# Kernel tuning notes

Hardware: AMD Instinct MI355X
Metric: run time of the kernel (lower is better)

## Reference

```python
import jax, jax.numpy as jnp
import numpy as np

N_NODES = 50000
N_EDGES = 640000
DIM = 128
BN_EPS = 1e-5
AGG_EPS = 1e-6


def setup_inputs() -> dict:
    key = jax.random.key(0)
    ks = jax.random.split(key, 32)
    s = 1.0 / np.sqrt(DIM)
    d = {}
    d["x"] = jax.random.normal(ks[0], (N_NODES, DIM), jnp.float32)
    d["e"] = jax.random.normal(ks[1], (N_EDGES, DIM), jnp.float32)
    # Linear layers A,B,C,D,E: weight [out,in], bias [out]
    for i, n in enumerate(["A", "B", "C", "D", "E"]):
        d[n + "w"] = jax.random.normal(ks[2 + 2 * i], (DIM, DIM), jnp.float32) * s
        d[n + "b"] = jax.random.normal(ks[3 + 2 * i], (DIM,), jnp.float32) * s
    # BatchNorm (eval mode) params / running stats for node and edge BN
    d["bn_x_gamma"] = 1.0 + 0.1 * jax.random.normal(ks[12], (DIM,), jnp.float32)
    d["bn_x_beta"] = 0.1 * jax.random.normal(ks[13], (DIM,), jnp.float32)
    d["bn_x_mean"] = 0.1 * jax.random.normal(ks[14], (DIM,), jnp.float32)
    d["bn_x_var"] = 0.5 + jax.random.uniform(ks[15], (DIM,), jnp.float32)
    d["bn_e_gamma"] = 1.0 + 0.1 * jax.random.normal(ks[16], (DIM,), jnp.float32)
    d["bn_e_beta"] = 0.1 * jax.random.normal(ks[17], (DIM,), jnp.float32)
    d["bn_e_mean"] = 0.1 * jax.random.normal(ks[18], (DIM,), jnp.float32)
    d["bn_e_var"] = 0.5 + jax.random.uniform(ks[19], (DIM,), jnp.float32)
    d["edge_index"] = jax.random.randint(ks[20], (2, N_EDGES), 0, N_NODES, dtype=jnp.int64)
    return d


def reference(x, e, Aw, Ab, Bw, Bb, Cw, Cb, Dw, Db, Ew, Eb,
              bn_x_gamma, bn_x_beta, bn_x_mean, bn_x_var,
              bn_e_gamma, bn_e_beta, bn_e_mean, bn_e_var,
              edge_index):
    # PyG default flow: x_j gathers from edge_index[0] (source),
    # x_i / aggregation index from edge_index[1] (target).
    src, dst = edge_index[0], edge_index[1]

    Ax = x @ Aw.T + Ab
    Bx = x @ Bw.T + Bb
    Ce = e @ Cw.T + Cb
    Dx = x @ Dw.T + Db
    Ex = x @ Ew.T + Eb

    # message: gated edge features
    e_ij = Dx[dst] + Ex[src] + Ce            # [n_edges, out_dim]
    sigma = jax.nn.sigmoid(e_ij)

    # aggregate: dual scatter-sum + divide
    num = jax.ops.segment_sum(sigma * Bx[src], dst, num_segments=N_NODES)
    den = jax.ops.segment_sum(sigma, dst, num_segments=N_NODES)
    aggr = num / (den + AGG_EPS)

    x_new = Ax + aggr                        # update()

    # BatchNorm (eval, running stats) + relu; dropout p=0 in eval
    x_bn = (x_new - bn_x_mean) * jax.lax.rsqrt(bn_x_var + BN_EPS) * bn_x_gamma + bn_x_beta
    e_bn = (e_ij - bn_e_mean) * jax.lax.rsqrt(bn_e_var + BN_EPS) * bn_e_gamma + bn_e_beta

    x_out = x + jax.nn.relu(x_bn)            # residual
    e_out = e + jax.nn.relu(e_bn)            # residual
    return x_out, e_out
```

## Files before the change

kernel.cpp:

```cpp
#include <hip/hip_runtime.h>
#include <hip/hip_bf16.h>
#include <math.h>

#define N_NODES 50000
#define N_EDGES 640000
#define DIM 128
#define LDP 136

typedef __attribute__((ext_vector_type(8))) short short8;
typedef __attribute__((ext_vector_type(4))) float floatx4;

__device__ __forceinline__ unsigned short f2bf(float f) {
    unsigned int u = __float_as_uint(f);
    u += 0x7FFFu + ((u >> 16) & 1u);
    return (unsigned short)(u >> 16);
}
__device__ __forceinline__ float bf2f(unsigned short h) {
    return __uint_as_float(((unsigned int)h) << 16);
}

__global__ __launch_bounds__(256) void node_gemm(
    const float* __restrict__ x,
    const float* __restrict__ w0, const float* __restrict__ b0,
    const float* __restrict__ w1, const float* __restrict__ b1,
    const float* __restrict__ w2, const float* __restrict__ b2,
    const float* __restrict__ w3, const float* __restrict__ b3,
    float* __restrict__ o0, float* __restrict__ o1,
    float* __restrict__ o2, float* __restrict__ o3)
{
    __shared__ unsigned short Xs[64 * LDP];
    __shared__ unsigned short Ws[128 * LDP];
    const int tid  = threadIdx.x;
    const int mblk = blockIdx.x * 64;
    const int mid  = blockIdx.y;
    const float* W = mid == 0 ? w0 : mid == 1 ? w1 : mid == 2 ? w2 : w3;
    const float* B = mid == 0 ? b0 : mid == 1 ? b1 : mid == 2 ? b2 : b3;
    float*       O = mid == 0 ? o0 : mid == 1 ? o1 : mid == 2 ? o2 : o3;

#pragma unroll
    for (int i = 0; i < 8; ++i) {
        int slot = tid + i * 256;
        int row = slot >> 5, c4 = (slot & 31) << 2;
        int rg = mblk + row;
        float4 v = make_float4(0.f, 0.f, 0.f, 0.f);
        if (rg < N_NODES) v = *(const float4*)(x + (size_t)rg * DIM + c4);
        unsigned short* p = &Xs[row * LDP + c4];
        p[0] = f2bf(v.x); p[1] = f2bf(v.y); p[2] = f2bf(v.z); p[3] = f2bf(v.w);
    }
#pragma unroll
    for (int i = 0; i < 16; ++i) {
        int slot = tid + i * 256;
        int row = slot >> 5, c4 = (slot & 31) << 2;
        float4 v = *(const float4*)(W + row * DIM + c4);
        unsigned short* p = &Ws[row * LDP + c4];
        p[0] = f2bf(v.x); p[1] = f2bf(v.y); p[2] = f2bf(v.z); p[3] = f2bf(v.w);
    }
    __syncthreads();

    const int wave = tid >> 6, lane = tid & 63;
    const int q = lane >> 4, r = lane & 15;
    floatx4 acc[8];
#pragma unroll
    for (int i = 0; i < 8; ++i) acc[i] = (floatx4)(0.f);
    const int arow = wave * 16 + r;
#pragma unroll
    for (int kk = 0; kk < 4; ++kk) {
        short8 a = *(const short8*)&Xs[arow * LDP + kk * 32 + q * 8];
#pragma unroll
        for (int nt = 0; nt < 8; ++nt) {
            short8 b = *(const short8*)&Ws[(nt * 16 + r) * LDP + kk * 32 + q * 8];
            acc[nt] = __builtin_amdgcn_mfma_f32_16x16x32_bf16(a, b, acc[nt], 0, 0, 0);
        }
    }
#pragma unroll
    for (int nt = 0; nt < 8; ++nt) {
        int col = nt * 16 + r;
        float bv = B[col];
#pragma unroll
        for (int reg = 0; reg < 4; ++reg) {
            int rg = mblk + wave * 16 + q * 4 + reg;
            if (rg < N_NODES) O[(size_t)rg * DIM + col] = acc[nt][reg] + bv;
        }
    }
}

__global__ __launch_bounds__(256) void edge_kernel(
    const float* __restrict__ e,
    const float* __restrict__ Cw, const float* __restrict__ Cb,
    const int* __restrict__ ei,
    const float* __restrict__ Dx, const float* __restrict__ Ex,
    const float* __restrict__ Bx,
    const float* __restrict__ g,  const float* __restrict__ bt,
    const float* __restrict__ mn, const float* __restrict__ vr,
    float* __restrict__ num, float* __restrict__ den,
    float* __restrict__ e_out)
{
    __shared__ unsigned short Es[64 * LDP];
    __shared__ unsigned short Ws[128 * LDP];
    __shared__ int srcS[64], dstS[64];
    const int tid  = threadIdx.x;
    const int mblk = blockIdx.x * 64;

    if (tid < 64) {
        srcS[tid] = ei[mblk + tid];
        dstS[tid] = ei[N_EDGES + mblk + tid];
    }
#pragma unroll
    for (int i = 0; i < 8; ++i) {
        int slot = tid + i * 256;
        int row = slot >> 5, c4 = (slot & 31) << 2;
        float4 v = *(const float4*)(e + (size_t)(mblk + row) * DIM + c4);
        unsigned short* p = &Es[row * LDP + c4];
        p[0] = f2bf(v.x); p[1] = f2bf(v.y); p[2] = f2bf(v.z); p[3] = f2bf(v.w);
    }
#pragma unroll
    for (int i = 0; i < 16; ++i) {
        int slot = tid + i * 256;
        int row = slot >> 5, c4 = (slot & 31) << 2;
        float4 v = *(const float4*)(Cw + row * DIM + c4);
        unsigned short* p = &Ws[row * LDP + c4];
        p[0] = f2bf(v.x); p[1] = f2bf(v.y); p[2] = f2bf(v.z); p[3] = f2bf(v.w);
    }
    __syncthreads();

    const int wave = tid >> 6, lane = tid & 63;
    const int q = lane >> 4, r = lane & 15;
    floatx4 acc[8];
#pragma unroll
    for (int i = 0; i < 8; ++i) acc[i] = (floatx4)(0.f);
    const int arow = wave * 16 + r;
#pragma unroll
    for (int kk = 0; kk < 4; ++kk) {
        short8 a = *(const short8*)&Es[arow * LDP + kk * 32 + q * 8];
#pragma unroll
        for (int nt = 0; nt < 8; ++nt) {
            short8 b = *(const short8*)&Ws[(nt * 16 + r) * LDP + kk * 32 + q * 8];
            acc[nt] = __builtin_amdgcn_mfma_f32_16x16x32_bf16(a, b, acc[nt], 0, 0, 0);
        }
    }

#pragma unroll
    for (int nt = 0; nt < 8; ++nt) {
        int col = nt * 16 + r;
        float cb = Cb[col];
        float sc = g[col] * rsqrtf(vr[col] + 1e-5f);
        float sh = bt[col] - mn[col] * sc;
#pragma unroll
        for (int reg = 0; reg < 4; ++reg) {
            int rl = wave * 16 + q * 4 + reg;
            int rg = mblk + rl;
            int dd = dstS[rl], ss = srcS[rl];
            float eij = acc[nt][reg] + cb
                      + Dx[(size_t)dd * DIM + col] + Ex[(size_t)ss * DIM + col];
            float sg = 1.f / (1.f + __expf(-eij));
            atomicAdd(&num[(size_t)dd * DIM + col], sg * Bx[(size_t)ss * DIM + col]);
            atomicAdd(&den[(size_t)dd * DIM + col], sg);
            float bn = eij * sc + sh;
            e_out[(size_t)rg * DIM + col] = bf2f(Es[rl * LDP + col]) + (bn > 0.f ? bn : 0.f);
        }
    }
}

__global__ __launch_bounds__(256) void node_final(
    const float* __restrict__ x,  const float* __restrict__ Ax,
    const float* __restrict__ num, const float* __restrict__ den,
    const float* __restrict__ g,  const float* __restrict__ bt,
    const float* __restrict__ mn, const float* __restrict__ vr,
    float* __restrict__ x_out)
{
    int idx = (blockIdx.x * 256 + threadIdx.x) * 4;
    float4 a  = *(const float4*)(Ax + idx);
    float4 nm = *(const float4*)(num + idx);
    float4 dn = *(const float4*)(den + idx);
    float4 xv = *(const float4*)(x + idx);
    int col = idx & (DIM - 1);
    float av[4] = {a.x, a.y, a.z, a.w};
    float nv[4] = {nm.x, nm.y, nm.z, nm.w};
    float dv[4] = {dn.x, dn.y, dn.z, dn.w};
    float xs[4] = {xv.x, xv.y, xv.z, xv.w};
    float ov[4];
#pragma unroll
    for (int j = 0; j < 4; ++j) {
        float sc = g[col + j] * rsqrtf(vr[col + j] + 1e-5f);
        float sh = bt[col + j] - mn[col + j] * sc;
        float v = av[j] + nv[j] / (dv[j] + 1e-6f);
        float bn = v * sc + sh;
        ov[j] = xs[j] + (bn > 0.f ? bn : 0.f);
    }
    *(float4*)(x_out + idx) = make_float4(ov[0], ov[1], ov[2], ov[3]);
}

extern "C" void kernel_launch(void* const* d_in, const int* in_sizes, int n_in,
                              void* d_out, int out_size, void* d_ws, size_t ws_size,
                              hipStream_t stream) {
    const float* x  = (const float*)d_in[0];
    const float* e  = (const float*)d_in[1];
    const float* Aw = (const float*)d_in[2];  const float* Ab = (const float*)d_in[3];
    const float* Bw = (const float*)d_in[4];  const float* Bb = (const float*)d_in[5];
    const float* Cw = (const float*)d_in[6];  const float* Cb = (const float*)d_in[7];
    const float* Dw = (const float*)d_in[8];  const float* Db = (const float*)d_in[9];
    const float* Ew = (const float*)d_in[10]; const float* Eb = (const float*)d_in[11];
    const float* gx = (const float*)d_in[12]; const float* btx = (const float*)d_in[13];
    const float* mnx = (const float*)d_in[14]; const float* vrx = (const float*)d_in[15];
    const float* ge = (const float*)d_in[16]; const float* bte = (const float*)d_in[17];
    const float* mne = (const float*)d_in[18]; const float* vre = (const float*)d_in[19];
    const int*   ei = (const int*)d_in[20];

    const size_t NF = (size_t)N_NODES * DIM;
    float* ws  = (float*)d_ws;
    float* Ax  = ws;
    float* Bx  = ws + NF;
    float* Dx  = ws + 2 * NF;
    float* Ex  = ws + 3 * NF;
    float* num = ws + 4 * NF;
    float* den = ws + 5 * NF;

    float* x_out = (float*)d_out;
    float* e_out = x_out + NF;

    hipMemsetAsync(num, 0, 2 * NF * sizeof(float), stream);

    dim3 g1((N_NODES + 63) / 64, 4);
    node_gemm<<<g1, 256, 0, stream>>>(x, Aw, Ab, Bw, Bb, Dw, Db, Ew, Eb, Ax, Bx, Dx, Ex);

    edge_kernel<<<N_EDGES / 64, 256, 0, stream>>>(e, Cw, Cb, ei, Dx, Ex, Bx,
                                                  ge, bte, mne, vre, num, den, e_out);

    node_final<<<(int)(NF / 4 / 256), 256, 0, stream>>>(x, Ax, num, den,
                                                        gx, btx, mnx, vrx, x_out);
}
```

Measured before the change: 1.206 ms.

## Replace atomic scatter-sum with CSR gather aggregation and pre-converted bf16 operands

Builds a destination-sorted CSR (histogram, scan, position assignment) so the edge kernel writes sigmoid values to sorted slots. A per-node kernel then gathers and reduces numerator and denominator without float atomics. It also pre-converts x and the weights to bf16 once. The trade-off is an extra large sigma buffer in workspace, several extra small kernels, and a fallback to the old atomic path when the workspace is too small.

```diff
diff --git a/kernel.cpp b/kernel.cpp
--- a/kernel.cpp
+++ b/kernel.cpp
@@ -19,7 +19,282 @@
     return __uint_as_float(((unsigned int)h) << 16);
 }
 
-__global__ __launch_bounds__(256) void node_gemm(
+
+__global__ __launch_bounds__(256) void convert_x(
+    const float* __restrict__ x, unsigned short* __restrict__ xb)
+{
+    size_t i = (size_t)(blockIdx.x * 256 + threadIdx.x) * 8;
+    float4 a = *(const float4*)(x + i);
+    float4 b = *(const float4*)(x + i + 4);
+    short8 v;
+    v[0] = (short)f2bf(a.x); v[1] = (short)f2bf(a.y);
+    v[2] = (short)f2bf(a.z); v[3] = (short)f2bf(a.w);
+    v[4] = (short)f2bf(b.x); v[5] = (short)f2bf(b.y);
+    v[6] = (short)f2bf(b.z); v[7] = (short)f2bf(b.w);
+    *(short8*)(xb + i) = v;
+}
+
+__global__ __launch_bounds__(256) void convert_w(
+    const float* __restrict__ w0, const float* __restrict__ w1,
+    const float* __restrict__ w2, const float* __restrict__ w3,
+    const float* __restrict__ w4, unsigned short* __restrict__ wb)
+{
+    const float* W = blockIdx.y == 0 ? w0 : blockIdx.y == 1 ? w1 :
+                     blockIdx.y == 2 ? w2 : blockIdx.y == 3 ? w3 : w4;
+    int i = (blockIdx.x * 256 + threadIdx.x) * 8;
+    float4 a = *(const float4*)(W + i);
+    float4 b = *(const float4*)(W + i + 4);
+    short8 v;
+    v[0] = (short)f2bf(a.x); v[1] = (short)f2bf(a.y);
+    v[2] = (short)f2bf(a.z); v[3] = (short)f2bf(a.w);
+    v[4] = (short)f2bf(b.x); v[5] = (short)f2bf(b.y);
+    v[6] = (short)f2bf(b.z); v[7] = (short)f2bf(b.w);
+    *(short8*)(wb + (size_t)blockIdx.y * DIM * DIM + i) = v;
+}
+
+__global__ __launch_bounds__(256) void hist_kernel(
+    const int* __restrict__ ei, int* __restrict__ deg)
+{
+    int e = blockIdx.x * 256 + threadIdx.x;
+    atomicAdd(&deg[ei[N_EDGES + e]], 1);
+}
+
+__global__ __launch_bounds__(256) void scan1(
+    const int* __restrict__ deg, int* __restrict__ off, int* __restrict__ bsum)
+{
+    __shared__ int s[256];
+    int tid = threadIdx.x;
+    int i = blockIdx.x * 256 + tid;
+    int v = (i < N_NODES) ? deg[i] : 0;
+    s[tid] = v;
+    __syncthreads();
+#pragma unroll
+    for (int d = 1; d < 256; d <<= 1) {
+        int t = (tid >= d) ? s[tid - d] : 0;
+        __syncthreads();
+        s[tid] += t;
+        __syncthreads();
+    }
+    if (i < N_NODES) off[i] = s[tid] - v;
+    if (tid == 255) bsum[blockIdx.x] = s[tid];
+}
+
+__global__ __launch_bounds__(256) void scan2(int* __restrict__ bsum)
+{
+    __shared__ int s[256];
+    int tid = threadIdx.x;
+    int v = (tid < 196) ? bsum[tid] : 0;
+    s[tid] = v;
+    __syncthreads();
+#pragma unroll
+    for (int d = 1; d < 256; d <<= 1) {
+        int t = (tid >= d) ? s[tid - d] : 0;
+        __syncthreads();
+        s[tid] += t;
+        __syncthreads();
+    }
+    if (tid < 196) bsum[tid] = s[tid] - v;
+}
+
+__global__ __launch_bounds__(256) void scan3(
+    int* __restrict__ off, const int* __restrict__ bsum, int* __restrict__ cursor)
+{
+    int i = blockIdx.x * 256 + threadIdx.x;
+    if (i < N_NODES) {
+        int o = off[i] + bsum[blockIdx.x];
+        off[i] = o;
+        cursor[i] = o;
+    }
+    if (i == 0) off[N_NODES] = N_EDGES;
+}
+
+__global__ __launch_bounds__(256) void pos_kernel(
+    const int* __restrict__ ei, int* __restrict__ cursor,
+    int* __restrict__ pos, int* __restrict__ srcp)
+{
+    int e = blockIdx.x * 256 + threadIdx.x;
+    int d = ei[N_EDGES + e];
+    int s = ei[e];
+    int p = atomicAdd(&cursor[d], 1);
+    pos[e] = p;
+    srcp[p] = s;
+}
+
+__global__ __launch_bounds__(256) void node_gemm_bf(
+    const unsigned short* __restrict__ xb, const unsigned short* __restrict__ wb,
+    const float* __restrict__ b0, const float* __restrict__ b1,
+    const float* __restrict__ b2, const float* __restrict__ b3,
+    float* __restrict__ o0, float* __restrict__ o1,
+    float* __restrict__ o2, float* __restrict__ o3)
+{
+    __shared__ unsigned short Xs[64 * LDP];
+    __shared__ unsigned short Ws[128 * LDP];
+    const int tid  = threadIdx.x;
+    const int mblk = blockIdx.x * 64;
+    const int mid  = blockIdx.y;
+    const int widx = (mid < 2) ? mid : mid + 1;
+    const unsigned short* Wm = wb + (size_t)widx * DIM * DIM;
+    const float* B = mid == 0 ? b0 : mid == 1 ? b1 : mid == 2 ? b2 : b3;
+    float*       O = mid == 0 ? o0 : mid == 1 ? o1 : mid == 2 ? o2 : o3;
+
+#pragma unroll
+    for (int i = 0; i < 4; ++i) {
+        int slot = tid + i * 256;
+        int row = slot >> 4, c8 = (slot & 15) << 3;
+        int rg = mblk + row;
+        short8 v = (short8)(0);
+        if (rg < N_NODES) v = *(const short8*)(xb + (size_t)rg * DIM + c8);
+        *(short8*)&Xs[row * LDP + c8] = v;
+    }
+#pragma unroll
+    for (int i = 0; i < 8; ++i) {
+        int slot = tid + i * 256;
+        int row = slot >> 4, c8 = (slot & 15) << 3;
+        *(short8*)&Ws[row * LDP + c8] = *(const short8*)(Wm + row * DIM + c8);
+    }
+    __syncthreads();
+
+    const int wave = tid >> 6, lane = tid & 63;
+    const int q = lane >> 4, r = lane & 15;
+    floatx4 acc[8];
+#pragma unroll
+    for (int i = 0; i < 8; ++i) acc[i] = (floatx4)(0.f);
+    const int arow = wave * 16 + r;
+#pragma unroll
+    for (int kk = 0; kk < 4; ++kk) {
+        short8 a = *(const short8*)&Xs[arow * LDP + kk * 32 + q * 8];
+#pragma unroll
+        for (int nt = 0; nt < 8; ++nt) {
+            short8 b = *(const short8*)&Ws[(nt * 16 + r) * LDP + kk * 32 + q * 8];
+            acc[nt] = __builtin_amdgcn_mfma_f32_16x16x32_bf16(a, b, acc[nt], 0, 0, 0);
+        }
+    }
+#pragma unroll
+    for (int nt = 0; nt < 8; ++nt) {
+        int col = nt * 16 + r;
+        float bv = B[col];
+#pragma unroll
+        for (int reg = 0; reg < 4; ++reg) {
+            int rg = mblk + wave * 16 + q * 4 + reg;
+            if (rg < N_NODES) O[(size_t)rg * DIM + col] = acc[nt][reg] + bv;
+        }
+    }
+}
+
+__global__ __launch_bounds__(256) void edge_kernel_v2(
+    const float* __restrict__ e,
+    const unsigned short* __restrict__ wb, const float* __restrict__ Cb,
+    const int* __restrict__ ei,
+    const float* __restrict__ Dx, const float* __restrict__ Ex,
+    const int* __restrict__ pos,
+    const float* __restrict__ g,  const float* __restrict__ bt,
+    const float* __restrict__ mn, const float* __restrict__ vr,
+    float* __restrict__ sigp, float* __restrict__ e_out)
+{
+    __shared__ unsigned short Es[64 * LDP];
+    __shared__ unsigned short Ws[128 * LDP];
+    __shared__ int srcS[64], dstS[64], posS[64];
+    const int tid  = threadIdx.x;
+    const int mblk = blockIdx.x * 64;
+
+    if (tid < 64) {
+        srcS[tid] = ei[mblk + tid];
+        dstS[tid] = ei[N_EDGES + mblk + tid];
+        posS[tid] = pos[mblk + tid];
+    }
+#pragma unroll
+    for (int i = 0; i < 8; ++i) {
+        int slot = tid + i * 256;
+        int row = slot >> 5, c4 = (slot & 31) << 2;
+        float4 v = *(const float4*)(e + (size_t)(mblk + row) * DIM + c4);
+        unsigned short* p = &Es[row * LDP + c4];
+        p[0] = f2bf(v.x); p[1] = f2bf(v.y); p[2] = f2bf(v.z); p[3] = f2bf(v.w);
+    }
+    const unsigned short* Wm = wb + (size_t)2 * DIM * DIM;
+#pragma unroll
+    for (int i = 0; i < 8; ++i) {
+        int slot = tid + i * 256;
+        int row = slot >> 4, c8 = (slot & 15) << 3;
+        *(short8*)&Ws[row * LDP + c8] = *(const short8*)(Wm + row * DIM + c8);
+    }
+    __syncthreads();
+
+    const int wave = tid >> 6, lane = tid & 63;
+    const int q = lane >> 4, r = lane & 15;
+    floatx4 acc[8];
+#pragma unroll
+    for (int i = 0; i < 8; ++i) acc[i] = (floatx4)(0.f);
+    const int arow = wave * 16 + r;
+#pragma unroll
+    for (int kk = 0; kk < 4; ++kk) {
+        short8 a = *(const short8*)&Es[arow * LDP + kk * 32 + q * 8];
+#pragma unroll
+        for (int nt = 0; nt < 8; ++nt) {
+            short8 b = *(const short8*)&Ws[(nt * 16 + r) * LDP + kk * 32 + q * 8];
+            acc[nt] = __builtin_amdgcn_mfma_f32_16x16x32_bf16(a, b, acc[nt], 0, 0, 0);
+        }
+    }
+
+#pragma unroll
+    for (int nt = 0; nt < 8; ++nt) {
+        int col = nt * 16 + r;
+        float cb = Cb[col];
+        float sc = g[col] * rsqrtf(vr[col] + 1e-5f);
+        float sh = bt[col] - mn[col] * sc;
+#pragma unroll
+        for (int reg = 0; reg < 4; ++reg) {
+            int rl = wave * 16 + q * 4 + reg;
+            int rg = mblk + rl;
+            int dd = dstS[rl], ss = srcS[rl];
+            float eij = acc[nt][reg] + cb
+                      + Dx[(size_t)dd * DIM + col] + Ex[(size_t)ss * DIM + col];
+            float sg = 1.f / (1.f + __expf(-eij));
+            sigp[(size_t)posS[rl] * DIM + col] = sg;
+            float bn = eij * sc + sh;
+            e_out[(size_t)rg * DIM + col] = bf2f(Es[rl * LDP + col]) + (bn > 0.f ? bn : 0.f);
+        }
+    }
+}
+
+__global__ __launch_bounds__(256) void node_aggr(
+    const float* __restrict__ x,  const float* __restrict__ Ax,
+    const float* __restrict__ Bx, const float* __restrict__ sigp,
+    const int* __restrict__ srcp, const int* __restrict__ off,
+    const float* __restrict__ g,  const float* __restrict__ bt,
+    const float* __restrict__ mn, const float* __restrict__ vr,
+    float* __restrict__ x_out)
+{
+    int node = blockIdx.x * 4 + (threadIdx.x >> 6);
+    int lane = threadIdx.x & 63;
+    int c0 = lane * 2;
+    int lo = off[node], hi = off[node + 1];
+    float n0 = 0.f, n1 = 0.f, d0 = 0.f, d1 = 0.f;
+    for (int k = lo; k < hi; ++k) {
+        float2 sg = *(const float2*)(sigp + (size_t)k * DIM + c0);
+        int s = srcp[k];
+        float2 bx = *(const float2*)(Bx + (size_t)s * DIM + c0);
+        n0 += sg.x * bx.x; n1 += sg.y * bx.y;
+        d0 += sg.x;        d1 += sg.y;
+    }
+    float2 gv  = *(const float2*)(g + c0);
+    float2 btv = *(const float2*)(bt + c0);
+    float2 mnv = *(const float2*)(mn + c0);
+    float2 vrv = *(const float2*)(vr + c0);
+    float2 av  = *(const float2*)(Ax + (size_t)node * DIM + c0);
+    float2 xv  = *(const float2*)(x  + (size_t)node * DIM + c0);
+    float sc0 = gv.x * rsqrtf(vrv.x + 1e-5f);
+    float sc1 = gv.y * rsqrtf(vrv.y + 1e-5f);
+    float v0 = av.x + n0 / (d0 + 1e-6f);
+    float v1 = av.y + n1 / (d1 + 1e-6f);
+    float bn0 = (v0 - mnv.x) * sc0 + btv.x;
+    float bn1 = (v1 - mnv.y) * sc1 + btv.y;
+    float2 o;
+    o.x = xv.x + (bn0 > 0.f ? bn0 : 0.f);
+    o.y = xv.y + (bn1 > 0.f ? bn1 : 0.f);
+    *(float2*)(x_out + (size_t)node * DIM + c0) = o;
+}
+
+__global__ __launch_bounds__(256) void node_gemm_old(
     const float* __restrict__ x,
     const float* __restrict__ w0, const float* __restrict__ b0,
     const float* __restrict__ w1, const float* __restrict__ b1,
@@ -84,7 +359,7 @@
     }
 }
 
-__global__ __launch_bounds__(256) void edge_kernel(
+__global__ __launch_bounds__(256) void edge_kernel_atomic(
     const float* __restrict__ e,
     const float* __restrict__ Cw, const float* __restrict__ Cb,
     const int* __restrict__ ei,
@@ -138,7 +413,6 @@
             acc[nt] = __builtin_amdgcn_mfma_f32_16x16x32_bf16(a, b, acc[nt], 0, 0, 0);
         }
     }
-
 #pragma unroll
     for (int nt = 0; nt < 8; ++nt) {
         int col = nt * 16 + r;
@@ -207,25 +481,66 @@
     const int*   ei = (const int*)d_in[20];
 
     const size_t NF = (size_t)N_NODES * DIM;
-    float* ws  = (float*)d_ws;
-    float* Ax  = ws;
-    float* Bx  = ws + NF;
-    float* Dx  = ws + 2 * NF;
-    float* Ex  = ws + 3 * NF;
-    float* num = ws + 4 * NF;
-    float* den = ws + 5 * NF;
+    const size_t EF = (size_t)N_EDGES * DIM;
 
     float* x_out = (float*)d_out;
     float* e_out = x_out + NF;
 
-    hipMemsetAsync(num, 0, 2 * NF * sizeof(float), stream);
-
-    dim3 g1((N_NODES + 63) / 64, 4);
-    node_gemm<<<g1, 256, 0, stream>>>(x, Aw, Ab, Bw, Bb, Dw, Db, Ew, Eb, Ax, Bx, Dx, Ex);
-
-    edge_kernel<<<N_EDGES / 64, 256, 0, stream>>>(e, Cw, Cb, ei, Dx, Ex, Bx,
-                                                  ge, bte, mne, vre, num, den, e_out);
-
-    node_final<<<(int)(NF / 4 / 256), 256, 0, stream>>>(x, Ax, num, den,
-                                                        gx, btx, mnx, vrx, x_out);
-}
+    char* base = (char*)d_ws;
+    size_t need = 0;
+    #define WS_ALLOC(ty, name, bytes) \
+        ty* name = (ty*)(base + need); need = (need + (size_t)(bytes) + 255) & ~(size_t)255;
+    WS_ALLOC(float, Ax, NF * 4)
+    WS_ALLOC(float, Bx, NF * 4)
+    WS_ALLOC(float, Dx, NF * 4)
+    WS_ALLOC(float, Ex, NF * 4)
+    WS_ALLOC(float, sigp, EF * 4)
+    WS_ALLOC(unsigned short, xb, NF * 2)
+    WS_ALLOC(unsigned short, wb, (size_t)5 * DIM * DIM * 2)
+    WS_ALLOC(int, deg, N_NODES * 4)
+    WS_ALLOC(int, offp, (N_NODES + 1) * 4)
+    WS_ALLOC(int, cursor, N_NODES * 4)
+    WS_ALLOC(int, bsum, 256 * 4)
+    WS_ALLOC(int, pos, N_EDGES * 4)
+    WS_ALLOC(int, srcp, N_EDGES * 4)
+    #undef WS_ALLOC
+
+    if (ws_size >= need) {
+        hipMemsetAsync(deg, 0, (size_t)N_NODES * 4, stream);
+        convert_x<<<3125, 256, 0, stream>>>(x, xb);
+        convert_w<<<dim3(8, 5), 256, 0, stream>>>(Aw, Bw, Cw, Dw, Ew, wb);
+
+        hist_kernel<<<N_EDGES / 256, 256, 0, stream>>>(ei, deg);
+        scan1<<<196, 256, 0, stream>>>(deg, offp, bsum);
+        scan2<<<1, 256, 0, stream>>>(bsum);
+        scan3<<<196, 256, 0, stream>>>(offp, bsum, cursor);
+        pos_kernel<<<N_EDGES / 256, 256, 0, stream>>>(ei, cursor, pos, srcp);
+
+        dim3 g1((N_NODES + 63) / 64, 4);
+        node_gemm_bf<<<g1, 256, 0, stream>>>(xb, wb, Ab, Bb, Db, Eb, Ax, Bx, Dx, Ex);
+
+        edge_kernel_v2<<<N_EDGES / 64, 256, 0, stream>>>(e, wb, Cb, ei, Dx, Ex, pos,
+                                                         ge, bte, mne, vre, sigp, e_out);
+
+        node_aggr<<<N_NODES / 4, 256, 0, stream>>>(x, Ax, Bx, sigp, srcp, offp,
+                                                   gx, btx, mnx, vrx, x_out);
+    } else {
+        float* ws  = (float*)d_ws;
+        float* fAx  = ws;
+        float* fBx  = ws + NF;
+        float* fDx  = ws + 2 * NF;
+        float* fEx  = ws + 3 * NF;
+        float* num = ws + 4 * NF;
+        float* den = ws + 5 * NF;
+
+        hipMemsetAsync(num, 0, 2 * NF * sizeof(float), stream);
+
+        dim3 g1((N_NODES + 63) / 64, 4);
+        node_gemm_old<<<g1, 256, 0, stream>>>(x, Aw, Ab, Bw, Bb, Dw, Db, Ew, Eb,
+                                              fAx, fBx, fDx, fEx);
+        edge_kernel_atomic<<<N_EDGES / 64, 256, 0, stream>>>(e, Cw, Cb, ei, fDx, fEx, fBx,
+                                                             ge, bte, mne, vre, num, den, e_out);
+        node_final<<<(int)(NF / 4 / 256), 256, 0, stream>>>(x, fAx, num, den,
+                                                            gx, btx, mnx, vrx, x_out);
+    }
+}
```

After: 1.045 ms. 13.3% less time.
